# Performance work log

Measured on AMD Instinct MI355X. Metric: run time of the kernel, lower is better.

Reference implementation:

```python
import jax, jax.numpy as jnp
import numpy as np

D_MODEL = 1024
NUM_HEADS = 16
D_K = D_MODEL // NUM_HEADS
D_FF = 4096
EPS = 1e-5


def layer_norm(x, gamma, beta):
    mu = jnp.mean(x, axis=-1, keepdims=True)
    var = jnp.mean(jnp.square(x - mu), axis=-1, keepdims=True)
    return (x - mu) * jax.lax.rsqrt(var + EPS) * gamma + beta


def setup_inputs() -> dict:
    key = jax.random.key(0)
    ks = jax.random.split(key, 12)
    B, S = 2, 2048
    s_attn = 1.0 / np.sqrt(D_MODEL)
    s_ff1 = 1.0 / np.sqrt(D_MODEL)
    s_ff2 = 1.0 / np.sqrt(D_FF)
    return {
        "x": jax.random.normal(ks[0], (B, S, D_MODEL), dtype=jnp.float32),
        "mask": jnp.ones((B, 1, 1, S), dtype=jnp.int32),
        "Wq": jax.random.normal(ks[1], (D_MODEL, D_MODEL), jnp.float32) * s_attn,
        "bq": jnp.zeros((D_MODEL,), jnp.float32),
        "Wk": jax.random.normal(ks[2], (D_MODEL, D_MODEL), jnp.float32) * s_attn,
        "bk": jnp.zeros((D_MODEL,), jnp.float32),
        "Wv": jax.random.normal(ks[3], (D_MODEL, D_MODEL), jnp.float32) * s_attn,
        "bv": jnp.zeros((D_MODEL,), jnp.float32),
        "Wo": jax.random.normal(ks[4], (D_MODEL, D_MODEL), jnp.float32) * s_attn,
        "bo": jnp.zeros((D_MODEL,), jnp.float32),
        "W1": jax.random.normal(ks[5], (D_MODEL, D_FF), jnp.float32) * s_ff1,
        "b1": jnp.zeros((D_FF,), jnp.float32),
        "W2": jax.random.normal(ks[6], (D_FF, D_MODEL), jnp.float32) * s_ff2,
        "b2": jnp.zeros((D_MODEL,), jnp.float32),
        "g1": jnp.ones((D_MODEL,), jnp.float32),
        "be1": jnp.zeros((D_MODEL,), jnp.float32),
        "g2": jnp.ones((D_MODEL,), jnp.float32),
        "be2": jnp.zeros((D_MODEL,), jnp.float32),
    }


def reference(x, mask, Wq, bq, Wk, bk, Wv, bv, Wo, bo, W1, b1, W2, b2, g1, be1, g2, be2):
    B, S, _ = x.shape

    def split_heads(t):  # [B,S,D] -> [B,H,S,Dk]
        return t.reshape(B, S, NUM_HEADS, D_K).transpose(0, 2, 1, 3)

    q = split_heads(x @ Wq + bq)
    k = split_heads(x @ Wk + bk)
    v = split_heads(x @ Wv + bv)

    scores = jnp.einsum("bhsd,bhtd->bhst", q, k) / np.sqrt(D_K)
    scores = jnp.where(mask == 0, -jnp.inf, scores)
    probs = jax.nn.softmax(scores, axis=-1)
    attn = jnp.einsum("bhst,bhtd->bhsd", probs, v)
    attn = attn.transpose(0, 2, 1, 3).reshape(B, S, D_MODEL)
    attn_out = attn @ Wo + bo

    h = layer_norm(x + attn_out, g1, be1)  # dropout=0 (eval)
    ff = jax.nn.relu(h @ W1 + b1) @ W2 + b2
    out = layer_norm(h + ff, g2, be2)
    return out
```

## Files before the change

kernel.cpp:

```cpp
#include <hip/hip_runtime.h>
#include <hip/hip_bf16.h>

#define DMODEL 1024
#define DFF    4096
#define NHEAD  16
#define DK     64
#define SEQ    2048
#define BATCH  2
#define MTOT   (BATCH*SEQ)
#define LOG2E  1.44269504f
#define MREF_L2E (-14.0f * 1.44269504f)

typedef __attribute__((ext_vector_type(8))) short bf16x8;
typedef __attribute__((ext_vector_type(4))) float f32x4;

typedef const unsigned int __attribute__((address_space(1)))* gas_u32p;
typedef unsigned int __attribute__((address_space(3)))* las_u32p;

__device__ __forceinline__ void gload_lds16(const void* g, void* l) {
  __builtin_amdgcn_global_load_lds((gas_u32p)g, (las_u32p)l, 16, 0, 0);
}

__device__ __forceinline__ f32x4 mfma16(bf16x8 a, bf16x8 b, f32x4 c) {
  return __builtin_amdgcn_mfma_f32_16x16x32_bf16(a, b, c, 0, 0, 0);
}

__device__ __forceinline__ unsigned short bf16bits(float f) {
  union { __hip_bfloat16 h; unsigned short u; } c; c.h = __float2bfloat16(f); return c.u;
}

__device__ __forceinline__ unsigned pack_bf16(float a, float b) {
  return (unsigned)bf16bits(a) | ((unsigned)bf16bits(b) << 16);
}

__device__ __forceinline__ void store_bf16x4(__hip_bfloat16* p, float a, float b, float c, float d) {
  union { __hip_bfloat16 h[4]; ushort4 u; } pk;
  pk.h[0] = __float2bfloat16(a); pk.h[1] = __float2bfloat16(b);
  pk.h[2] = __float2bfloat16(c); pk.h[3] = __float2bfloat16(d);
  *(ushort4*)p = pk.u;
}

__global__ __launch_bounds__(256) void cvt_bf16_kernel(const float* __restrict__ in,
                                                       __hip_bfloat16* __restrict__ out, int n) {
  int i = (blockIdx.x * 256 + threadIdx.x) * 4;
  if (i >= n) return;
  float4 v = *(const float4*)(in + i);
  store_bf16x4(out + i, v.x, v.y, v.z, v.w);
}

__global__ __launch_bounds__(256) void transpose_cvt_kernel(const float* __restrict__ in,
                                                            __hip_bfloat16* __restrict__ out,
                                                            int R, int C) {
  __shared__ float tile[32][33];
  int tx = threadIdx.x, ty = threadIdx.y;
  int c0 = blockIdx.x * 32, r0 = blockIdx.y * 32;
  #pragma unroll
  for (int j = 0; j < 32; j += 8)
    tile[ty + j][tx] = in[(size_t)(r0 + ty + j) * C + c0 + tx];
  __syncthreads();
  #pragma unroll
  for (int j = 0; j < 32; j += 8)
    out[(size_t)(c0 + ty + j) * R + r0 + tx] = __float2bfloat16(tile[tx][ty + j]);
}

__global__ __launch_bounds__(256)
void transpose4_cvt_kernel(const float* __restrict__ A0, const float* __restrict__ A1,
                           const float* __restrict__ A2, const float* __restrict__ A3,
                           __hip_bfloat16* __restrict__ O0, __hip_bfloat16* __restrict__ O1,
                           __hip_bfloat16* __restrict__ O2, __hip_bfloat16* __restrict__ O3) {
  const float* in; __hip_bfloat16* out;
  switch (blockIdx.z) {
    case 0: in = A0; out = O0; break;
    case 1: in = A1; out = O1; break;
    case 2: in = A2; out = O2; break;
    default: in = A3; out = O3; break;
  }
  __shared__ float tile[32][33];
  int tx = threadIdx.x, ty = threadIdx.y;
  int c0 = blockIdx.x * 32, r0 = blockIdx.y * 32;
  #pragma unroll
  for (int j = 0; j < 32; j += 8)
    tile[ty + j][tx] = in[(size_t)(r0 + ty + j) * DMODEL + c0 + tx];
  __syncthreads();
  #pragma unroll
  for (int j = 0; j < 32; j += 8)
    out[(size_t)(c0 + ty + j) * DMODEL + r0 + tx] = __float2bfloat16(tile[tx][ty + j]);
}

template<int MI, int NT>
__device__ __forceinline__ void gemm_core(const __hip_bfloat16* __restrict__ A,
                                          const __hip_bfloat16* __restrict__ Bt,
                                          int K, size_t blockM, size_t blockN,
                                          __hip_bfloat16* As, __hip_bfloat16* Bs,
                                          f32x4 (&acc)[MI][4]) {
  constexpr int BM = (NT / 128) * MI * 16;
  constexpr int RP = NT / 8;
  const int tid = threadIdx.x;
  const int w = tid >> 6, l = tid & 63;
  const int q = l >> 4, ln = l & 15;
  const int m_off = (w >> 1) * MI * 16, n_off = (w & 1) * 64;
  const int lr = l >> 3, lc = (l & 7) ^ lr;

  for (int k0 = 0; k0 < K; k0 += 64) {
    __syncthreads();
    #pragma unroll
    for (int t = 0; t < 128 / RP; ++t) {
      int ra = t * RP + w * 8;
      gload_lds16(Bt + (blockN + ra + lr) * (size_t)K + k0 + lc * 8, Bs + ra * 64);
      if (t < BM / RP)
        gload_lds16(A + (blockM + ra + lr) * (size_t)K + k0 + lc * 8, As + ra * 64);
    }
    __syncthreads();
    #pragma unroll
    for (int kk = 0; kk < 2; ++kk) {
      bf16x8 af[MI], bfr[4];
      #pragma unroll
      for (int mi = 0; mi < MI; ++mi) {
        int R = m_off + mi * 16 + ln;
        int p = (kk * 4 + q) ^ (R & 7);
        af[mi] = *(const bf16x8*)(As + R * 64 + p * 8);
      }
      #pragma unroll
      for (int ni = 0; ni < 4; ++ni) {
        int R = n_off + ni * 16 + ln;
        int p = (kk * 4 + q) ^ (R & 7);
        bfr[ni] = *(const bf16x8*)(Bs + R * 64 + p * 8);
      }
      #pragma unroll
      for (int mi = 0; mi < MI; ++mi)
        #pragma unroll
        for (int ni = 0; ni < 4; ++ni)
          acc[mi][ni] = mfma16(af[mi], bfr[ni], acc[mi][ni]);
    }
  }
}

template<int MI, int NT, int RELU, int WRITE_BF16>
__global__ __launch_bounds__(NT)
void gemm_bt_kernel(const __hip_bfloat16* __restrict__ A, const __hip_bfloat16* __restrict__ Bt,
                    const float* __restrict__ bias, float* __restrict__ Cf,
                    __hip_bfloat16* __restrict__ Cb, int M, int N, int K) {
  constexpr int BM = (NT / 128) * MI * 16;
  __shared__ __align__(16) __hip_bfloat16 As[BM * 64];
  __shared__ __align__(16) __hip_bfloat16 Bs[128 * 64];
  f32x4 acc[MI][4] = {};
  const size_t blockM = blockIdx.y * (size_t)BM, blockN = blockIdx.x * 128;
  gemm_core<MI, NT>(A, Bt, K, blockM, blockN, As, Bs, acc);

  const int tid = threadIdx.x;
  const int w = tid >> 6, l = tid & 63, q = l >> 4, ln = l & 15;
  const int m_off = (w >> 1) * MI * 16, n_off = (w & 1) * 64;
  #pragma unroll
  for (int ni = 0; ni < 4; ++ni) {
    size_t col = blockN + n_off + ni * 16 + ln;
    float bv = bias[col];
    #pragma unroll
    for (int mi = 0; mi < MI; ++mi) {
      size_t rowb = blockM + m_off + mi * 16 + q * 4;
      f32x4 v = acc[mi][ni];
      #pragma unroll
      for (int r = 0; r < 4; ++r) {
        float y = v[r] + bv;
        if (RELU) y = fmaxf(y, 0.0f);
        if (WRITE_BF16) Cb[(rowb + r) * N + col] = __float2bfloat16(y);
        else            Cf[(rowb + r) * N + col] = y;
      }
    }
  }
}

__global__ __launch_bounds__(256)
void gemm_qkv_kernel(const __hip_bfloat16* __restrict__ A, const __hip_bfloat16* __restrict__ Bt,
                     const float* __restrict__ bq, const float* __restrict__ bk,
                     const float* __restrict__ bv,
                     __hip_bfloat16* __restrict__ Qo, __hip_bfloat16* __restrict__ Ko,
                     __hip_bfloat16* __restrict__ VTo) {
  __shared__ __align__(16) __hip_bfloat16 As[128 * 64];
  __shared__ __align__(16) __hip_bfloat16 Bs[128 * 64];
  f32x4 acc[4][4] = {};
  const size_t blockM = blockIdx.y * 128, blockN = blockIdx.x * 128;
  const int sel = blockIdx.x >> 3;
  gemm_core<4, 256>(A, Bt, DMODEL, blockM, blockN, As, Bs, acc);

  const int tid = threadIdx.x;
  const int w = tid >> 6, l = tid & 63, q = l >> 4, ln = l & 15;
  const int m_off = (w >> 1) * 64, n_off = (w & 1) * 64;
  const int ncol0 = (int)blockN - sel * DMODEL;

  if (sel == 2) {
    #pragma unroll
    for (int ni = 0; ni < 4; ++ni) {
      int col = ncol0 + n_off + ni * 16 + ln;
      float bvv = bv[col];
      int hh = col >> 6, d = col & 63;
      #pragma unroll
      for (int mi = 0; mi < 4; ++mi) {
        size_t rowb = blockM + m_off + mi * 16 + q * 4;
        int bb = (int)(rowb >> 11), s = (int)(rowb & 2047);
        f32x4 v = acc[mi][ni];
        uint2 pk;
        pk.x = pack_bf16(v[0] + bvv, v[1] + bvv);
        pk.y = pack_bf16(v[2] + bvv, v[3] + bvv);
        *(uint2*)(VTo + (((size_t)(bb * NHEAD + hh) * DK + d) * SEQ + s)) = pk;
      }
    }
  } else {
    const float* bias = (sel == 0) ? bq : bk;
    const float scale = (sel == 0) ? 0.125f : 1.0f;
    __hip_bfloat16* outp = (sel == 0) ? Qo : Ko;
    #pragma unroll
    for (int ni = 0; ni < 4; ++ni) {
      int col = ncol0 + n_off + ni * 16 + ln;
      float bvv = bias[col];
      #pragma unroll
      for (int mi = 0; mi < 4; ++mi) {
        size_t rowb = blockM + m_off + mi * 16 + q * 4;
        f32x4 v = acc[mi][ni];
        #pragma unroll
        for (int r = 0; r < 4; ++r)
          outp[(rowb + r) * DMODEL + col] = __float2bfloat16((v[r] + bvv) * scale);
      }
    }
  }
}

__global__ __launch_bounds__(256, 2)
void attn_kernel(const __hip_bfloat16* __restrict__ Q, const __hip_bfloat16* __restrict__ Kg,
                 const __hip_bfloat16* __restrict__ VT, const int* __restrict__ mask,
                 __hip_bfloat16* __restrict__ Oout) {
  const int tid = threadIdx.x, w = tid >> 6, l = tid & 63, q = l >> 4, ln = l & 15;
  const int qt = blockIdx.x, h = blockIdx.y, b = blockIdx.z;
  const size_t wrow = (size_t)b * SEQ + qt * 128 + w * 32;
  const int hcol = h * DK;
  const __hip_bfloat16* vth = VT + ((size_t)(b * NHEAD + h)) * DK * SEQ;
  const __hip_bfloat16* kgb = Kg + (size_t)b * SEQ * DMODEL;
  const int* mk = mask + (size_t)b * SEQ;

  __shared__ __align__(16) __hip_bfloat16 Pb[4][32 * 64];
  __shared__ __align__(16) float maskL[SEQ];
  __hip_bfloat16* pw = &Pb[w][0];

  #pragma unroll
  for (int i = tid; i < SEQ / 4; i += 256) {
    int4 mv = ((const int4*)mk)[i];
    float4 mf;
    mf.x = mv.x ? MREF_L2E : -1e30f; mf.y = mv.y ? MREF_L2E : -1e30f;
    mf.z = mv.z ? MREF_L2E : -1e30f; mf.w = mv.w ? MREF_L2E : -1e30f;
    ((float4*)maskL)[i] = mf;
  }

  bf16x8 qf[2][2];
  #pragma unroll
  for (int mi = 0; mi < 2; ++mi)
    #pragma unroll
    for (int kc = 0; kc < 2; ++kc)
      qf[mi][kc] = *(const bf16x8*)(Q + (wrow + mi * 16 + ln) * DMODEL + hcol + kc * 32 + q * 8);

  __syncthreads();

  f32x4 Oacc[2][4] = {};
  float l_[2] = {0.f, 0.f};

  bf16x8 kfA[8], kfB[8];

  auto load_k = [&](bf16x8* kf, int kt) {
    #pragma unroll
    for (int t = 0; t < 4; ++t)
      #pragma unroll
      for (int kc = 0; kc < 2; ++kc)
        kf[t * 2 + kc] = *(const bf16x8*)(kgb + (size_t)(kt + t * 16 + ln) * DMODEL + hcol + kc * 32 + q * 8);
  };
  auto load_v = [&](bf16x8* vf, int kt) {
    #pragma unroll
    for (int ni = 0; ni < 4; ++ni)
      #pragma unroll
      for (int kc = 0; kc < 2; ++kc)
        vf[ni * 2 + kc] = *(const bf16x8*)(vth + (size_t)(ni * 16 + ln) * SEQ + kt + kc * 32 + q * 8);
  };
  auto compute = [&](const bf16x8* kf, const bf16x8* vf, int kt) {
    f32x4 st[2][4] = {};
    #pragma unroll
    for (int kc = 0; kc < 2; ++kc)
      #pragma unroll
      for (int mi = 0; mi < 2; ++mi)
        #pragma unroll
        for (int t = 0; t < 4; ++t)
          st[mi][t] = mfma16(kf[t * 2 + kc], qf[mi][kc], st[mi][t]);
    #pragma unroll
    for (int mi = 0; mi < 2; ++mi) {
      float rs = 0.f;
      #pragma unroll
      for (int t = 0; t < 4; ++t) {
        f32x4 mb = *(const f32x4*)(maskL + kt + t * 16 + q * 4);
        float p0 = __builtin_amdgcn_exp2f(__builtin_fmaf(st[mi][t][0], LOG2E, mb[0]));
        float p1 = __builtin_amdgcn_exp2f(__builtin_fmaf(st[mi][t][1], LOG2E, mb[1]));
        float p2 = __builtin_amdgcn_exp2f(__builtin_fmaf(st[mi][t][2], LOG2E, mb[2]));
        float p3 = __builtin_amdgcn_exp2f(__builtin_fmaf(st[mi][t][3], LOG2E, mb[3]));
        rs += (p0 + p1) + (p2 + p3);
        uint2 pk; pk.x = pack_bf16(p0, p1); pk.y = pack_bf16(p2, p3);
        int cs = 2 * t + (q >> 1);
        *(uint2*)(pw + (mi * 16 + ln) * 64 + ((cs ^ (ln & 7)) << 3) + (q & 1) * 4) = pk;
      }
      l_[mi] += rs;
    }
    #pragma unroll
    for (int kc = 0; kc < 2; ++kc) {
      bf16x8 pf[2];
      #pragma unroll
      for (int mi = 0; mi < 2; ++mi)
        pf[mi] = *(const bf16x8*)(pw + (mi * 16 + ln) * 64 + (((kc * 4 + q) ^ (ln & 7)) << 3));
      #pragma unroll
      for (int mi = 0; mi < 2; ++mi)
        #pragma unroll
        for (int ni = 0; ni < 4; ++ni)
          Oacc[mi][ni] = mfma16(pf[mi], vf[ni * 2 + kc], Oacc[mi][ni]);
    }
  };

  load_k(kfA, 0);
  for (int kt = 0; kt < SEQ; kt += 128) {
    {
      bf16x8 vf[8];
      load_v(vf, kt);
      load_k(kfB, kt + 64);
      compute(kfA, vf, kt);
    }
    {
      bf16x8 vf[8];
      load_v(vf, kt + 64);
      if (kt + 128 < SEQ) load_k(kfA, kt + 128);
      compute(kfB, vf, kt + 64);
    }
  }

  #pragma unroll
  for (int mi = 0; mi < 2; ++mi) {
    l_[mi] += __shfl_xor(l_[mi], 16);
    l_[mi] += __shfl_xor(l_[mi], 32);
  }
  #pragma unroll
  for (int mi = 0; mi < 2; ++mi) {
    float inv = 1.0f / l_[mi];
    f32x4 i4;
    #pragma unroll
    for (int r = 0; r < 4; ++r) i4[r] = __shfl(inv, (l & 48) + q * 4 + r);
    #pragma unroll
    for (int ni = 0; ni < 4; ++ni)
      #pragma unroll
      for (int r = 0; r < 4; ++r)
        Oout[(wrow + mi * 16 + q * 4 + r) * DMODEL + hcol + ni * 16 + ln] =
            __float2bfloat16(Oacc[mi][ni][r] * i4[r]);
  }
}

__global__ __launch_bounds__(256)
void add_ln_kernel(const float* __restrict__ X, const float* __restrict__ Y,
                   const float* __restrict__ gam, const float* __restrict__ bet,
                   float* __restrict__ Of, __hip_bfloat16* __restrict__ Ob) {
  int row = blockIdx.x, tid = threadIdx.x;
  const float4 a = *(const float4*)(X + (size_t)row * DMODEL + tid * 4);
  const float4 c = *(const float4*)(Y + (size_t)row * DMODEL + tid * 4);
  float v0 = a.x + c.x, v1 = a.y + c.y, v2 = a.z + c.z, v3 = a.w + c.w;
  float s  = v0 + v1 + v2 + v3;
  float s2 = v0 * v0 + v1 * v1 + v2 * v2 + v3 * v3;
  #pragma unroll
  for (int off = 1; off < 64; off <<= 1) {
    s  += __shfl_xor(s, off);
    s2 += __shfl_xor(s2, off);
  }
  __shared__ float red[8];
  int w = tid >> 6, l = tid & 63;
  if (l == 0) { red[w] = s; red[4 + w] = s2; }
  __syncthreads();
  float S1 = red[0] + red[1] + red[2] + red[3];
  float S2 = red[4] + red[5] + red[6] + red[7];
  float mu = S1 * (1.0f / DMODEL);
  float var = S2 * (1.0f / DMODEL) - mu * mu;
  float rstd = rsqrtf(var + 1e-5f);
  const float4 gv = *(const float4*)(gam + tid * 4);
  const float4 bv = *(const float4*)(bet + tid * 4);
  float y0 = (v0 - mu) * rstd * gv.x + bv.x;
  float y1 = (v1 - mu) * rstd * gv.y + bv.y;
  float y2 = (v2 - mu) * rstd * gv.z + bv.z;
  float y3 = (v3 - mu) * rstd * gv.w + bv.w;
  float4 ov = {y0, y1, y2, y3};
  *(float4*)(Of + (size_t)row * DMODEL + tid * 4) = ov;
  if (Ob) store_bf16x4(Ob + (size_t)row * DMODEL + tid * 4, y0, y1, y2, y3);
}

extern "C" void kernel_launch(void* const* d_in, const int* in_sizes, int n_in,
                              void* d_out, int out_size, void* d_ws, size_t ws_size,
                              hipStream_t stream) {
  const float* x    = (const float*)d_in[0];
  const int*   mask = (const int*)d_in[1];
  const float* Wq = (const float*)d_in[2];  const float* bq = (const float*)d_in[3];
  const float* Wk = (const float*)d_in[4];  const float* bk = (const float*)d_in[5];
  const float* Wv = (const float*)d_in[6];  const float* bv = (const float*)d_in[7];
  const float* Wo = (const float*)d_in[8];  const float* bo = (const float*)d_in[9];
  const float* W1 = (const float*)d_in[10]; const float* b1 = (const float*)d_in[11];
  const float* W2 = (const float*)d_in[12]; const float* b2 = (const float*)d_in[13];
  const float* g1 = (const float*)d_in[14]; const float* be1 = (const float*)d_in[15];
  const float* g2 = (const float*)d_in[16]; const float* be2 = (const float*)d_in[17];
  float* out = (float*)d_out;

  char* ws = (char*)d_ws;
  const size_t MB = 1024ull * 1024ull;
  __hip_bfloat16* xb   = (__hip_bfloat16*)(ws + 0 * MB);
  __hip_bfloat16* WqT  = (__hip_bfloat16*)(ws + 8 * MB);
  __hip_bfloat16* WkT  = (__hip_bfloat16*)(ws + 10 * MB);
  __hip_bfloat16* WvT  = (__hip_bfloat16*)(ws + 12 * MB);
  __hip_bfloat16* WoT  = (__hip_bfloat16*)(ws + 14 * MB);
  __hip_bfloat16* W1T  = (__hip_bfloat16*)(ws + 16 * MB);
  __hip_bfloat16* W2T  = (__hip_bfloat16*)(ws + 24 * MB);
  __hip_bfloat16* Qb   = (__hip_bfloat16*)(ws + 32 * MB);
  __hip_bfloat16* Kb   = (__hip_bfloat16*)(ws + 40 * MB);
  __hip_bfloat16* VTb  = (__hip_bfloat16*)(ws + 48 * MB);
  __hip_bfloat16* attnB= (__hip_bfloat16*)(ws + 56 * MB);
  float*          AO   = (float*)(ws + 32 * MB);
  float*          hbuf = (float*)(ws + 48 * MB);
  __hip_bfloat16* hb   = (__hip_bfloat16*)(ws + 64 * MB);
  __hip_bfloat16* ff1  = (__hip_bfloat16*)(ws + 72 * MB);
  float*          ff2  = (float*)(ws + 32 * MB);

  dim3 blk256(256);
  dim3 blkT(32, 8);

  cvt_bf16_kernel<<<dim3(4096), blk256, 0, stream>>>(x, xb, MTOT * DMODEL);
  transpose4_cvt_kernel<<<dim3(32, 32, 4), blkT, 0, stream>>>(Wq, Wk, Wv, Wo, WqT, WkT, WvT, WoT);
  transpose_cvt_kernel<<<dim3(128, 32), blkT, 0, stream>>>(W1, W1T, DMODEL, DFF);
  transpose_cvt_kernel<<<dim3(32, 128), blkT, 0, stream>>>(W2, W2T, DFF, DMODEL);

  gemm_qkv_kernel<<<dim3(24, 32), blk256, 0, stream>>>(xb, WqT, bq, bk, bv, Qb, Kb, VTb);

  attn_kernel<<<dim3(16, 16, 2), blk256, 0, stream>>>(Qb, Kb, VTb, mask, attnB);

  gemm_bt_kernel<2, 256, 0, 0><<<dim3(8, 64), blk256, 0, stream>>>(attnB, WoT, bo, AO, nullptr, MTOT, DMODEL, DMODEL);

  add_ln_kernel<<<dim3(MTOT), blk256, 0, stream>>>(x, AO, g1, be1, hbuf, hb);

  gemm_bt_kernel<4, 256, 1, 1><<<dim3(32, 32), blk256, 0, stream>>>(hb, W1T, b1, nullptr, ff1, MTOT, DFF, DMODEL);

  gemm_bt_kernel<2, 256, 0, 0><<<dim3(8, 64), blk256, 0, stream>>>(ff1, W2T, b2, ff2, nullptr, MTOT, DMODEL, DFF);

  add_ln_kernel<<<dim3(MTOT), blk256, 0, stream>>>(hbuf, ff2, g2, be2, out, nullptr);
}
```

Before: 440.2 us.

## Split attention over the key dimension and reduce partials in a separate kernel

The attention kernel now splits each query tile's key range into two halves, launching twice as many blocks. Each block writes unnormalized fp32 partial outputs and row sums to workspace. A new reduce kernel adds the halves, normalizes, and writes bf16. This raises parallelism from 512 blocks and raises the occupancy hint to 4 blocks per SU. The cost is an extra launch and about 32MB of fp32 partial traffic. The split is valid without max rescaling because the softmax uses a fixed reference offset instead of a running max.

```diff
diff --git a/kernel.cpp b/kernel.cpp
--- a/kernel.cpp
+++ b/kernel.cpp
@@ -10,6 +10,8 @@
 #define MTOT   (BATCH*SEQ)
 #define LOG2E  1.44269504f
 #define MREF_L2E (-14.0f * 1.44269504f)
+#define KSPLIT 2
+#define KSEQ   (SEQ / KSPLIT)
 
 typedef __attribute__((ext_vector_type(8))) short bf16x8;
 typedef __attribute__((ext_vector_type(4))) float f32x4;
@@ -224,29 +226,30 @@
   }
 }
 
-__global__ __launch_bounds__(256, 2)
+__global__ __launch_bounds__(256, 4)
 void attn_kernel(const __hip_bfloat16* __restrict__ Q, const __hip_bfloat16* __restrict__ Kg,
                  const __hip_bfloat16* __restrict__ VT, const int* __restrict__ mask,
-                 __hip_bfloat16* __restrict__ Oout) {
+                 float* __restrict__ Opart, float* __restrict__ Lpart) {
   const int tid = threadIdx.x, w = tid >> 6, l = tid & 63, q = l >> 4, ln = l & 15;
-  const int qt = blockIdx.x, h = blockIdx.y, b = blockIdx.z;
+  const int qt = blockIdx.x, h = blockIdx.y;
+  const int b = blockIdx.z >> 1, sp = blockIdx.z & 1;
+  const int kb = sp * KSEQ;
   const size_t wrow = (size_t)b * SEQ + qt * 128 + w * 32;
   const int hcol = h * DK;
   const __hip_bfloat16* vth = VT + ((size_t)(b * NHEAD + h)) * DK * SEQ;
   const __hip_bfloat16* kgb = Kg + (size_t)b * SEQ * DMODEL;
-  const int* mk = mask + (size_t)b * SEQ;
+  const int* mk = mask + (size_t)b * SEQ + kb;
 
   __shared__ __align__(16) __hip_bfloat16 Pb[4][32 * 64];
-  __shared__ __align__(16) float maskL[SEQ];
+  __shared__ __align__(16) float maskL[KSEQ];
   __hip_bfloat16* pw = &Pb[w][0];
 
-  #pragma unroll
-  for (int i = tid; i < SEQ / 4; i += 256) {
-    int4 mv = ((const int4*)mk)[i];
+  {
+    int4 mv = ((const int4*)mk)[tid];
     float4 mf;
     mf.x = mv.x ? MREF_L2E : -1e30f; mf.y = mv.y ? MREF_L2E : -1e30f;
     mf.z = mv.z ? MREF_L2E : -1e30f; mf.w = mv.w ? MREF_L2E : -1e30f;
-    ((float4*)maskL)[i] = mf;
+    ((float4*)maskL)[tid] = mf;
   }
 
   bf16x8 qf[2][2];
@@ -291,7 +294,7 @@
       float rs = 0.f;
       #pragma unroll
       for (int t = 0; t < 4; ++t) {
-        f32x4 mb = *(const f32x4*)(maskL + kt + t * 16 + q * 4);
+        f32x4 mb = *(const f32x4*)(maskL + (kt - kb) + t * 16 + q * 4);
         float p0 = __builtin_amdgcn_exp2f(__builtin_fmaf(st[mi][t][0], LOG2E, mb[0]));
         float p1 = __builtin_amdgcn_exp2f(__builtin_fmaf(st[mi][t][1], LOG2E, mb[1]));
         float p2 = __builtin_amdgcn_exp2f(__builtin_fmaf(st[mi][t][2], LOG2E, mb[2]));
@@ -317,8 +320,8 @@
     }
   };
 
-  load_k(kfA, 0);
-  for (int kt = 0; kt < SEQ; kt += 128) {
+  load_k(kfA, kb);
+  for (int kt = kb; kt < kb + KSEQ; kt += 128) {
     {
       bf16x8 vf[8];
       load_v(vf, kt);
@@ -328,7 +331,7 @@
     {
       bf16x8 vf[8];
       load_v(vf, kt + 64);
-      if (kt + 128 < SEQ) load_k(kfA, kt + 128);
+      if (kt + 128 < kb + KSEQ) load_k(kfA, kt + 128);
       compute(kfB, vf, kt + 64);
     }
   }
@@ -338,19 +341,32 @@
     l_[mi] += __shfl_xor(l_[mi], 16);
     l_[mi] += __shfl_xor(l_[mi], 32);
   }
+  float* op = Opart + (size_t)sp * MTOT * DMODEL;
   #pragma unroll
   for (int mi = 0; mi < 2; ++mi) {
-    float inv = 1.0f / l_[mi];
-    f32x4 i4;
-    #pragma unroll
-    for (int r = 0; r < 4; ++r) i4[r] = __shfl(inv, (l & 48) + q * 4 + r);
     #pragma unroll
     for (int ni = 0; ni < 4; ++ni)
       #pragma unroll
       for (int r = 0; r < 4; ++r)
-        Oout[(wrow + mi * 16 + q * 4 + r) * DMODEL + hcol + ni * 16 + ln] =
-            __float2bfloat16(Oacc[mi][ni][r] * i4[r]);
-  }
+        op[(wrow + mi * 16 + q * 4 + r) * DMODEL + hcol + ni * 16 + ln] = Oacc[mi][ni][r];
+    if (l < 16)
+      Lpart[((size_t)sp * MTOT + wrow + mi * 16 + l) * NHEAD + h] = l_[mi];
+  }
+}
+
+__global__ __launch_bounds__(256)
+void attn_reduce_kernel(const float* __restrict__ Opart, const float* __restrict__ Lpart,
+                        __hip_bfloat16* __restrict__ Oout) {
+  const int row = blockIdx.x, tid = threadIdx.x;
+  const int col = tid * 4, h = col >> 6;
+  float l0 = Lpart[(size_t)row * NHEAD + h];
+  float l1 = Lpart[((size_t)MTOT + row) * NHEAD + h];
+  float inv = 1.0f / (l0 + l1);
+  float4 o0 = *(const float4*)(Opart + (size_t)row * DMODEL + col);
+  float4 o1 = *(const float4*)(Opart + ((size_t)MTOT + row) * DMODEL + col);
+  store_bf16x4(Oout + (size_t)row * DMODEL + col,
+               (o0.x + o1.x) * inv, (o0.y + o1.y) * inv,
+               (o0.z + o1.z) * inv, (o0.w + o1.w) * inv);
 }
 
 __global__ __launch_bounds__(256)
@@ -416,6 +432,8 @@
   __hip_bfloat16* Kb   = (__hip_bfloat16*)(ws + 40 * MB);
   __hip_bfloat16* VTb  = (__hip_bfloat16*)(ws + 48 * MB);
   __hip_bfloat16* attnB= (__hip_bfloat16*)(ws + 56 * MB);
+  float*          Lpart= (float*)(ws + 0 * MB);
+  float*          Opart= (float*)(ws + 72 * MB);
   float*          AO   = (float*)(ws + 32 * MB);
   float*          hbuf = (float*)(ws + 48 * MB);
   __hip_bfloat16* hb   = (__hip_bfloat16*)(ws + 64 * MB);
@@ -432,7 +450,8 @@
 
   gemm_qkv_kernel<<<dim3(24, 32), blk256, 0, stream>>>(xb, WqT, bq, bk, bv, Qb, Kb, VTb);
 
-  attn_kernel<<<dim3(16, 16, 2), blk256, 0, stream>>>(Qb, Kb, VTb, mask, attnB);
+  attn_kernel<<<dim3(16, 16, 2 * KSPLIT), blk256, 0, stream>>>(Qb, Kb, VTb, mask, Opart, Lpart);
+  attn_reduce_kernel<<<dim3(MTOT), blk256, 0, stream>>>(Opart, Lpart, attnB);
 
   gemm_bt_kernel<2, 256, 0, 0><<<dim3(8, 64), blk256, 0, stream>>>(attnB, WoT, bo, AO, nullptr, MTOT, DMODEL, DMODEL);
 
```

Measured after the change: 731.1 us. +66.1%, slower.
